# Kernel optimization log

Measured on AMD Instinct MI355X. Metric: run time of the kernel, lower is better.

The kernel has to match this reference:

```python
import jax, jax.numpy as jnp
import numpy as np

B, N, E = 2, 2048, 1024
HQ, HKV = 16, 4           # query heads, kv heads
G = HQ // HKV             # groups (== HKV by construction; required by source einsum)
D = E // HQ               # head_dim = 64
KV_E = D * HKV            # kv projection dim = 256
LN_EPS = 1e-5


def _layernorm(x, g, b):
    mu = jnp.mean(x, axis=-1, keepdims=True)
    var = jnp.mean(jnp.square(x - mu), axis=-1, keepdims=True)
    return (x - mu) * jax.lax.rsqrt(var + LN_EPS) * g + b


def setup_inputs() -> dict:
    key = jax.random.key(0)
    ks = jax.random.split(key, 5)
    s = 0.02
    return {
        "x": jax.random.normal(ks[0], (B, N, E), dtype=jnp.float32),
        "Wq": jax.random.normal(ks[1], (E, E), dtype=jnp.float32) * s,
        "Wk": jax.random.normal(ks[2], (E, KV_E), dtype=jnp.float32) * s,
        "Wv": jax.random.normal(ks[3], (E, KV_E), dtype=jnp.float32) * s,
        "Wout": jax.random.normal(ks[4], (E, E), dtype=jnp.float32) * s,
        "ln_g": jnp.ones((E,), dtype=jnp.float32),
        "ln_b": jnp.zeros((E,), dtype=jnp.float32),
    }


def reference(x, Wq, Wk, Wv, Wout, ln_g, ln_b):
    b, n, _ = x.shape
    # projections
    q = (x @ Wq).reshape(b, n, HQ, D).transpose(0, 2, 1, 3)   # b hq n d
    k = (x @ Wk).reshape(b, n, HKV, D).transpose(0, 2, 1, 3)  # b hkv s d
    v = (x @ Wv).reshape(b, n, HKV, D).transpose(0, 2, 1, 3)  # b hkv s d
    # split query heads: (h g) with h=HKV outer, g=G inner -> b hkv g n d
    q = q.reshape(b, HKV, G, n, D)
    scale = jnp.asarray(np.sqrt(D), dtype=x.dtype)
    scores = jnp.einsum('bhgnd,bhsd->bhgns', q, k) / scale    # b hkv g n s
    causal = jnp.tril(jnp.ones((n, n), dtype=bool))           # n s
    scores = jnp.where(causal[None, None, None, :, :], scores, jnp.asarray(-jnp.inf, x.dtype))
    attn = jax.nn.softmax(scores, axis=-1)                    # b i=hkv j=g n s
    # Faithful to source's mislabeled einsum: value head axis is indexed by the
    # GROUP index j (valid because G == HKV here).
    out = jnp.einsum('bijns,bjsd->bijnd', attn, v)            # b i j n d
    # rearrange 'b g h n d -> b n (h g) d' with g=i, h=j -> merged head order (j, i)
    out = out.transpose(0, 3, 2, 1, 4).reshape(b, n, HQ * D)  # b n E
    out = _layernorm(out, ln_g, ln_b) @ Wout
    # rearrange 'b g h n s -> b n s (h g)' then mean over n
    attn_w = attn.transpose(0, 3, 4, 2, 1).reshape(b, n, n, HQ).mean(axis=1)  # b s HQ
    return (out, attn_w)
```

## Files before the change

### kernel.cpp

```cpp
#include <hip/hip_runtime.h>

#define BB 2
#define NN 2048
#define EE 1024
#define HQH 16
#define DD 64
#define KVE 256
#define QKVW 1536

typedef short bf16x8 __attribute__((ext_vector_type(8)));
typedef short bf16x4 __attribute__((ext_vector_type(4)));
typedef float f32x4 __attribute__((ext_vector_type(4)));
typedef unsigned short u16;
typedef unsigned int u32;

#if __has_builtin(__builtin_amdgcn_exp2f)
#define EXP2(x) __builtin_amdgcn_exp2f(x)
#else
#define EXP2(x) exp2f(x)
#endif

#define QSCALE 0.18033688011112042f

__device__ __forceinline__ u16 f2bf(float f) {
    unsigned u = __float_as_uint(f);
    u += 0x7FFFu + ((u >> 16) & 1u);
    return (u16)(u >> 16);
}
__device__ __forceinline__ float bf2f(u16 h) {
    return __uint_as_float(((unsigned)h) << 16);
}
__device__ __forceinline__ u32 cvtpk(float a, float b) {
    u32 r;
    asm("v_cvt_pk_bf16_f32 %0, %1, %2" : "=v"(r) : "v"(a), "v"(b));
    return r;
}

#define GLOAD_LDS16(gp, lp) __builtin_amdgcn_global_load_lds( \
    (const __attribute__((address_space(1))) unsigned int*)(gp), \
    (__attribute__((address_space(3))) unsigned int*)(lp), 16, 0, 0)

__device__ __forceinline__ bf16x8 xpose8(bf16x8 v, int q) {
    union { bf16x8 v; u32 r[4]; } u_;
    u_.v = v;
    u32 r0 = u_.r[0], r1 = u_.r[1], r2 = u_.r[2], r3 = u_.r[3];
    u32 x, y, t0;
    x = (q & 4) ? r0 : r2;  y = (q & 4) ? r1 : r3;
    x = __shfl_xor(x, 4);   y = __shfl_xor(y, 4);
    if (q & 4) { r0 = x; r1 = y; } else { r2 = x; r3 = y; }
    x = (q & 2) ? r0 : r1;  y = (q & 2) ? r2 : r3;
    x = __shfl_xor(x, 2);   y = __shfl_xor(y, 2);
    if (q & 2) { r0 = x; r2 = y; } else { r1 = x; r3 = y; }
    t0 = __shfl_xor(r0, 1); r0 = (q & 1) ? ((t0 >> 16) | (r0 & 0xFFFF0000u)) : ((r0 & 0xFFFFu) | (t0 << 16));
    t0 = __shfl_xor(r1, 1); r1 = (q & 1) ? ((t0 >> 16) | (r1 & 0xFFFF0000u)) : ((r1 & 0xFFFFu) | (t0 << 16));
    t0 = __shfl_xor(r2, 1); r2 = (q & 1) ? ((t0 >> 16) | (r2 & 0xFFFF0000u)) : ((r2 & 0xFFFFu) | (t0 << 16));
    t0 = __shfl_xor(r3, 1); r3 = (q & 1) ? ((t0 >> 16) | (r3 & 0xFFFF0000u)) : ((r3 & 0xFFFFu) | (t0 << 16));
    u_.r[0] = r0; u_.r[1] = r1; u_.r[2] = r2; u_.r[3] = r3;
    return u_.v;
}

__global__ __launch_bounds__(256)
void conv_bf16(const float* __restrict__ in, u16* __restrict__ out) {
    int i = (blockIdx.x * 256 + threadIdx.x) * 8;
    float4 a = *(const float4*)&in[i];
    float4 b = *(const float4*)&in[i + 4];
    bf16x8 p;
    p[0] = f2bf(a.x); p[1] = f2bf(a.y); p[2] = f2bf(a.z); p[3] = f2bf(a.w);
    p[4] = f2bf(b.x); p[5] = f2bf(b.y); p[6] = f2bf(b.z); p[7] = f2bf(b.w);
    *(bf16x8*)&out[i] = p;
}

__global__ __launch_bounds__(256)
void transp_bf16(const float* __restrict__ W, u16* __restrict__ WT, int Nc) {
    __shared__ float tile[32][33];
    int k0 = blockIdx.x * 32, n0 = blockIdx.y * 32;
    int tx = threadIdx.x & 31, ty = threadIdx.x >> 5;
#pragma unroll
    for (int i = 0; i < 4; ++i)
        tile[ty + i * 8][tx] = W[(size_t)(k0 + ty + i * 8) * Nc + n0 + tx];
    __syncthreads();
#pragma unroll
    for (int i = 0; i < 4; ++i)
        WT[(size_t)(n0 + ty + i * 8) * EE + k0 + tx] = f2bf(tile[tx][ty + i * 8]);
}

__global__ __launch_bounds__(256)
void gemm_mfma(const u16* __restrict__ A, const u16* __restrict__ BT,
               void* __restrict__ C, int K, int ldc, int obf16,
               float qscale, int nq) {
    __shared__ __attribute__((aligned(16))) u16 sA[128 * 64];
    __shared__ __attribute__((aligned(16))) u16 sB[128 * 64];
    int t = threadIdx.x;
    int lane = t & 63, w = t >> 6;
    int wr = w >> 1, wc = w & 1;
    int l15 = lane & 15, lg = lane >> 4;
    int m0 = blockIdx.y * 128, n0 = blockIdx.x * 128;

    f32x4 acc[4][4];
#pragma unroll
    for (int mi = 0; mi < 4; ++mi)
#pragma unroll
        for (int ni = 0; ni < 4; ++ni) acc[mi][ni] = (f32x4){0.f, 0.f, 0.f, 0.f};

    int srow = lane >> 3;
    int schunk = (lane & 7) ^ srow;
    const u16* ga = A + (size_t)(m0 + w * 32 + srow) * K + schunk * 8;
    const u16* gb = BT + (size_t)(n0 + w * 32 + srow) * K + schunk * 8;
    char* lA = (char*)sA + w * 4096;
    char* lB = (char*)sB + w * 4096;

    for (int k0 = 0; k0 < K; k0 += 64) {
#pragma unroll
        for (int i = 0; i < 4; ++i) {
            GLOAD_LDS16(ga + (size_t)i * 8 * K + k0, lA + i * 1024);
            GLOAD_LDS16(gb + (size_t)i * 8 * K + k0, lB + i * 1024);
        }
        __syncthreads();
#pragma unroll
        for (int ks = 0; ks < 2; ++ks) {
            bf16x8 af[4], bfr[4];
#pragma unroll
            for (int mi = 0; mi < 4; ++mi) {
                int row = wr * 64 + mi * 16 + l15;
                af[mi] = *(const bf16x8*)((char*)sA +
                    ((row * 128 + lg * 16 + ks * 64) ^ ((row & 7) << 4)));
            }
#pragma unroll
            for (int ni = 0; ni < 4; ++ni) {
                int row = wc * 64 + ni * 16 + l15;
                bfr[ni] = *(const bf16x8*)((char*)sB +
                    ((row * 128 + lg * 16 + ks * 64) ^ ((row & 7) << 4)));
            }
#pragma unroll
            for (int mi = 0; mi < 4; ++mi)
#pragma unroll
                for (int ni = 0; ni < 4; ++ni)
                    acc[mi][ni] = __builtin_amdgcn_mfma_f32_16x16x32_bf16(
                        af[mi], bfr[ni], acc[mi][ni], 0, 0, 0);
        }
        __syncthreads();
    }

#pragma unroll
    for (int mi = 0; mi < 4; ++mi) {
        int rbase = m0 + wr * 64 + mi * 16 + lg * 4;
#pragma unroll
        for (int ni = 0; ni < 4; ++ni) {
            int col = n0 + wc * 64 + ni * 16 + l15;
            float sc = (col < nq) ? qscale : 1.0f;
            if (obf16) {
                u16* Cb = (u16*)C;
#pragma unroll
                for (int r = 0; r < 4; ++r)
                    Cb[(size_t)(rbase + r) * ldc + col] = f2bf(acc[mi][ni][r] * sc);
            } else {
                float* Cf = (float*)C;
#pragma unroll
                for (int r = 0; r < 4; ++r)
                    Cf[(size_t)(rbase + r) * ldc + col] = acc[mi][ni][r] * sc;
            }
        }
    }
}

__global__ __launch_bounds__(256)
void flash_attn(const u16* __restrict__ QKV, u16* __restrict__ AOb,
                float* __restrict__ mbuf, float* __restrict__ lbuf) {
    __shared__ __attribute__((aligned(16))) u16 sV[2][64 * 64];

    int blk = blockIdx.x;
    int ntile = 15 - (blk & 15);
    int bh = blk >> 4;
    int hq = bh & 15;
    int b = bh >> 4;
    int ih = hq >> 2, jh = hq & 3;
    int hm = jh * 4 + ih;
    int n0 = ntile * 128;
    int t = threadIdx.x;
    int lane = t & 63, w = t >> 6;
    int l15 = lane & 15, lg = lane >> 4;
    int q8 = t & 7;

    const u16* Kg = QKV + (size_t)b * NN * QKVW + EE + ih * DD;
    const u16* Vg = QKV + (size_t)b * NN * QKVW + EE + KVE + jh * DD;

    bf16x8 qf[2][2];
#pragma unroll
    for (int tt = 0; tt < 2; ++tt)
#pragma unroll
        for (int h = 0; h < 2; ++h)
            qf[tt][h] = *(const bf16x8*)(QKV +
                (size_t)(b * NN + n0 + w * 32 + tt * 16 + l15) * QKVW + hq * DD + lg * 8 + h * 32);

    f32x4 o[2][4];
    float mrow[2] = {-1e30f, -1e30f};
    float lrow[2] = {0.f, 0.f};
#pragma unroll
    for (int tt = 0; tt < 2; ++tt)
#pragma unroll
        for (int i = 0; i < 4; ++i) o[tt][i] = (f32x4){0.f, 0.f, 0.f, 0.f};

    int nt = (n0 + 128) >> 6;
    bf16x8 vr[2];
#pragma unroll
    for (int it = 0; it < 2; ++it) {
        int lin = t + it * 256;
        vr[it] = *(const bf16x8*)(Vg + (size_t)((lin >> 6) * 8 + q8) * QKVW + ((lin >> 3) & 7) * 8);
    }
#pragma unroll
    for (int it = 0; it < 2; ++it) {
        int lin = t + it * 256;
        int d = ((lin >> 3) & 7) * 8 + q8;
        int sbase = (lin >> 6) * 8;
        bf16x8 vt = xpose8(vr[it], q8);
        *(bf16x8*)((char*)sV[0] + ((d * 128 + sbase * 2) ^ (q8 << 4))) = vt;
    }

    for (int ti = 0; ti < nt; ++ti) {
        int s0 = ti << 6;
        if (ti + 1 < nt) {
#pragma unroll
            for (int it = 0; it < 2; ++it) {
                int lin = t + it * 256;
                vr[it] = *(const bf16x8*)(Vg +
                    (size_t)(s0 + 64 + (lin >> 6) * 8 + q8) * QKVW + ((lin >> 3) & 7) * 8);
            }
        }
        __syncthreads();
        const char* vb = (const char*)sV[ti & 1];

        f32x4 sf[2][4];
#pragma unroll
        for (int sub = 0; sub < 4; ++sub) {
            const u16* kp = Kg + (size_t)(s0 + sub * 16 + l15) * QKVW + lg * 8;
            bf16x8 k0 = *(const bf16x8*)kp;
            bf16x8 k1 = *(const bf16x8*)(kp + 32);
#pragma unroll
            for (int tt = 0; tt < 2; ++tt) {
                f32x4 z = {0.f, 0.f, 0.f, 0.f};
                z = __builtin_amdgcn_mfma_f32_16x16x32_bf16(k0, qf[tt][0], z, 0, 0, 0);
                sf[tt][sub] = __builtin_amdgcn_mfma_f32_16x16x32_bf16(k1, qf[tt][1], z, 0, 0, 0);
            }
        }

        bf16x8 vf[4][2];
#pragma unroll
        for (int sd = 0; sd < 4; ++sd) {
            int d = sd * 16 + l15;
            int swz = (d & 7) << 4;
#pragma unroll
            for (int f = 0; f < 2; ++f) {
                int aA = (d * 128 + (f * 32 + lg * 4) * 2) ^ swz;
                int aB = (d * 128 + (f * 32 + 16 + lg * 4) * 2) ^ swz;
                bf16x4 lo = *(const bf16x4*)(vb + aA);
                bf16x4 hi = *(const bf16x4*)(vb + aB);
                bf16x8 vv;
                vv[0] = lo[0]; vv[1] = lo[1]; vv[2] = lo[2]; vv[3] = lo[3];
                vv[4] = hi[0]; vv[5] = hi[1]; vv[6] = hi[2]; vv[7] = hi[3];
                vf[sd][f] = vv;
            }
        }

#pragma unroll
        for (int tt = 0; tt < 2; ++tt) {
            int ng_min = n0 + w * 32 + tt * 16;
            int ng = ng_min + l15;
            float mcur = -1e30f;
            if (s0 + 63 > ng_min) {
#pragma unroll
                for (int sub = 0; sub < 4; ++sub)
#pragma unroll
                    for (int r = 0; r < 4; ++r) {
                        int sg = s0 + sub * 16 + lg * 4 + r;
                        float sc = (sg <= ng) ? sf[tt][sub][r] : -1e30f;
                        sf[tt][sub][r] = sc;
                        mcur = fmaxf(mcur, sc);
                    }
            } else {
#pragma unroll
                for (int sub = 0; sub < 4; ++sub)
#pragma unroll
                    for (int r = 0; r < 4; ++r) mcur = fmaxf(mcur, sf[tt][sub][r]);
            }
            mcur = fmaxf(mcur, __shfl_xor(mcur, 16));
            mcur = fmaxf(mcur, __shfl_xor(mcur, 32));

            float mn = mrow[tt];
            if (!__all(mcur <= mn + 8.0f)) {
                mn = fmaxf(mn, mcur);
                float alpha = EXP2(mrow[tt] - mn);
                mrow[tt] = mn;
                lrow[tt] *= alpha;
                float a0 = __shfl(alpha, lg * 4 + 0);
                float a1 = __shfl(alpha, lg * 4 + 1);
                float a2 = __shfl(alpha, lg * 4 + 2);
                float a3 = __shfl(alpha, lg * 4 + 3);
#pragma unroll
                for (int sd = 0; sd < 4; ++sd) {
                    o[tt][sd][0] *= a0; o[tt][sd][1] *= a1;
                    o[tt][sd][2] *= a2; o[tt][sd][3] *= a3;
                }
            }
            float rs = 0.f;
#pragma unroll
            for (int sub = 0; sub < 4; ++sub)
#pragma unroll
                for (int r = 0; r < 4; ++r) {
                    float p = EXP2(sf[tt][sub][r] - mn);
                    sf[tt][sub][r] = p;
                    rs += p;
                }
            rs += __shfl_xor(rs, 16);
            rs += __shfl_xor(rs, 32);
            lrow[tt] += rs;

            union { u32 r[4]; bf16x8 v; } pa0, pa1;
            pa0.r[0] = cvtpk(sf[tt][0][0], sf[tt][0][1]);
            pa0.r[1] = cvtpk(sf[tt][0][2], sf[tt][0][3]);
            pa0.r[2] = cvtpk(sf[tt][1][0], sf[tt][1][1]);
            pa0.r[3] = cvtpk(sf[tt][1][2], sf[tt][1][3]);
            pa1.r[0] = cvtpk(sf[tt][2][0], sf[tt][2][1]);
            pa1.r[1] = cvtpk(sf[tt][2][2], sf[tt][2][3]);
            pa1.r[2] = cvtpk(sf[tt][3][0], sf[tt][3][1]);
            pa1.r[3] = cvtpk(sf[tt][3][2], sf[tt][3][3]);
#pragma unroll
            for (int sd = 0; sd < 4; ++sd) {
                o[tt][sd] = __builtin_amdgcn_mfma_f32_16x16x32_bf16(pa0.v, vf[sd][0], o[tt][sd], 0, 0, 0);
                o[tt][sd] = __builtin_amdgcn_mfma_f32_16x16x32_bf16(pa1.v, vf[sd][1], o[tt][sd], 0, 0, 0);
            }
        }

        if (ti + 1 < nt) {
#pragma unroll
            for (int it = 0; it < 2; ++it) {
                int lin = t + it * 256;
                int d = ((lin >> 3) & 7) * 8 + q8;
                int sbase = (lin >> 6) * 8;
                bf16x8 vt = xpose8(vr[it], q8);
                *(bf16x8*)((char*)sV[(ti + 1) & 1] + ((d * 128 + sbase * 2) ^ (q8 << 4))) = vt;
            }
        }
    }

#pragma unroll
    for (int tt = 0; tt < 2; ++tt) {
        float linv = 1.f / lrow[tt];
        if (lg == 0) {
            int n = n0 + w * 32 + tt * 16 + l15;
            mbuf[(size_t)bh * NN + n] = mrow[tt];
            lbuf[(size_t)bh * NN + n] = linv;
        }
        float i0 = __shfl(linv, lg * 4 + 0);
        float i1 = __shfl(linv, lg * 4 + 1);
        float i2 = __shfl(linv, lg * 4 + 2);
        float i3 = __shfl(linv, lg * 4 + 3);
#pragma unroll
        for (int sd = 0; sd < 4; ++sd) {
            int nb = n0 + w * 32 + tt * 16 + lg * 4;
            size_t base = (size_t)(b * NN + nb) * EE + hm * DD + sd * 16 + l15;
            AOb[base]          = f2bf(o[tt][sd][0] * i0);
            AOb[base + EE]     = f2bf(o[tt][sd][1] * i1);
            AOb[base + 2 * EE] = f2bf(o[tt][sd][2] * i2);
            AOb[base + 3 * EE] = f2bf(o[tt][sd][3] * i3);
        }
    }
}

__global__ __launch_bounds__(256)
void colsum_mfma(const u16* __restrict__ QKV,
                 const float* __restrict__ mbuf, const float* __restrict__ lbuf,
                 float* __restrict__ AW) {
    int blk = blockIdx.x;
    int stile = blk & 15;
    int bh = blk >> 4;
    int hq = bh & 15;
    int b = bh >> 4;
    int ih = hq >> 2, jh = hq & 3;
    int hm = jh * 4 + ih;
    int t = threadIdx.x;
    int lane = t & 63, w = t >> 6;
    int l15 = lane & 15, lg = lane >> 4;
    int sb = stile * 128 + w * 32;

    bf16x8 kf[2][2];
#pragma unroll
    for (int st = 0; st < 2; ++st)
#pragma unroll
        for (int h = 0; h < 2; ++h)
            kf[st][h] = *(const bf16x8*)(QKV +
                (size_t)(b * NN + sb + st * 16 + l15) * QKVW + EE + ih * DD + lg * 8 + h * 32);

    float acc[2][4] = {};
    int nstart = stile * 128;

    const u16* qp0 = QKV + (size_t)(b * NN + nstart + l15) * QKVW + hq * DD + lg * 8;
    bf16x8 q0 = *(const bf16x8*)qp0;
    bf16x8 q1 = *(const bf16x8*)(qp0 + 32);
    float mv = mbuf[(size_t)bh * NN + nstart + l15];
    float li = lbuf[(size_t)bh * NN + nstart + l15];

    for (int nn0 = nstart; nn0 < NN; nn0 += 16) {
        bf16x8 cq0 = q0, cq1 = q1;
        float cmv = mv, cli = li;
        if (nn0 + 16 < NN) {
            const u16* qp = QKV + (size_t)(b * NN + nn0 + 16 + l15) * QKVW + hq * DD + lg * 8;
            q0 = *(const bf16x8*)qp;
            q1 = *(const bf16x8*)(qp + 32);
            mv = mbuf[(size_t)bh * NN + nn0 + 16 + l15];
            li = lbuf[(size_t)bh * NN + nn0 + 16 + l15];
        }
        int n = nn0 + l15;
#pragma unroll
        for (int st = 0; st < 2; ++st) {
            f32x4 z = {0.f, 0.f, 0.f, 0.f};
            z = __builtin_amdgcn_mfma_f32_16x16x32_bf16(kf[st][0], cq0, z, 0, 0, 0);
            z = __builtin_amdgcn_mfma_f32_16x16x32_bf16(kf[st][1], cq1, z, 0, 0, 0);
#pragma unroll
            for (int r = 0; r < 4; ++r) {
                int s = sb + st * 16 + lg * 4 + r;
                float val = EXP2(z[r] - cmv) * cli;
                acc[st][r] += (n >= s) ? val : 0.f;
            }
        }
    }
#pragma unroll
    for (int st = 0; st < 2; ++st)
#pragma unroll
        for (int r = 0; r < 4; ++r) {
            float a = acc[st][r];
            a += __shfl_xor(a, 1);
            a += __shfl_xor(a, 2);
            a += __shfl_xor(a, 4);
            a += __shfl_xor(a, 8);
            if (l15 == 0) {
                int s = sb + st * 16 + lg * 4 + r;
                AW[((size_t)b * NN + s) * HQH + hm] = a * (1.0f / NN);
            }
        }
}

__global__ __launch_bounds__(256)
void layernorm_bf16(u16* __restrict__ X, const float* __restrict__ g,
                    const float* __restrict__ bt) {
    __shared__ float red[256];
    int row = blockIdx.x;
    int t = threadIdx.x;
    u16* xp = X + (size_t)row * EE;
    ushort4 v = *(ushort4*)&xp[t * 4];
    float x0 = bf2f(v.x), x1 = bf2f(v.y), x2 = bf2f(v.z), x3 = bf2f(v.w);
    red[t] = x0 + x1 + x2 + x3;
    __syncthreads();
    for (int off = 128; off > 0; off >>= 1) {
        if (t < off) red[t] += red[t + off];
        __syncthreads();
    }
    float mu = red[0] * (1.f / EE);
    __syncthreads();
    float d0 = x0 - mu, d1 = x1 - mu, d2 = x2 - mu, d3 = x3 - mu;
    red[t] = d0 * d0 + d1 * d1 + d2 * d2 + d3 * d3;
    __syncthreads();
    for (int off = 128; off > 0; off >>= 1) {
        if (t < off) red[t] += red[t + off];
        __syncthreads();
    }
    float rstd = rsqrtf(red[0] * (1.f / EE) + 1e-5f);
    float4 gg = *(const float4*)&g[t * 4];
    float4 bb = *(const float4*)&bt[t * 4];
    ushort4 o;
    o.x = f2bf(d0 * rstd * gg.x + bb.x);
    o.y = f2bf(d1 * rstd * gg.y + bb.y);
    o.z = f2bf(d2 * rstd * gg.z + bb.z);
    o.w = f2bf(d3 * rstd * gg.w + bb.w);
    *(ushort4*)&xp[t * 4] = o;
}

extern "C" void kernel_launch(void* const* d_in, const int* in_sizes, int n_in,
                              void* d_out, int out_size, void* d_ws, size_t ws_size,
                              hipStream_t stream) {
    const float* x    = (const float*)d_in[0];
    const float* Wq   = (const float*)d_in[1];
    const float* Wk   = (const float*)d_in[2];
    const float* Wv   = (const float*)d_in[3];
    const float* Wout = (const float*)d_in[4];
    const float* lng  = (const float*)d_in[5];
    const float* lnb  = (const float*)d_in[6];

    float* out = (float*)d_out;
    float* aw  = out + (size_t)BB * NN * EE;

    u16* Xb    = (u16*)d_ws;
    u16* QKVb  = Xb + (size_t)BB * NN * EE;
    u16* WqkvT = QKVb + (size_t)BB * NN * QKVW;
    u16* WoutT = WqkvT + (size_t)QKVW * EE;
    u16* AOb   = WoutT + (size_t)EE * EE;
    float* mb  = (float*)(AOb + (size_t)BB * NN * EE);
    float* lb  = mb + (size_t)BB * HQH * NN;

    dim3 blk(256);

    conv_bf16<<<BB * NN * EE / 2048, blk, 0, stream>>>(x, Xb);
    transp_bf16<<<dim3(32, 32), blk, 0, stream>>>(Wq, WqkvT, EE);
    transp_bf16<<<dim3(32, 8), blk, 0, stream>>>(Wk, WqkvT + (size_t)EE * EE, KVE);
    transp_bf16<<<dim3(32, 8), blk, 0, stream>>>(Wv, WqkvT + (size_t)(EE + KVE) * EE, KVE);
    transp_bf16<<<dim3(32, 32), blk, 0, stream>>>(Wout, WoutT, EE);

    gemm_mfma<<<dim3(QKVW / 128, BB * NN / 128), blk, 0, stream>>>(
        Xb, WqkvT, QKVb, EE, QKVW, 1, QSCALE, EE);

    int ablocks = BB * HQH * 16;
    flash_attn<<<ablocks, blk, 0, stream>>>(QKVb, AOb, mb, lb);
    colsum_mfma<<<ablocks, blk, 0, stream>>>(QKVb, mb, lb, aw);

    layernorm_bf16<<<BB * NN, blk, 0, stream>>>(AOb, lng, lnb);

    gemm_mfma<<<dim3(EE / 128, BB * NN / 128), blk, 0, stream>>>(
        AOb, WoutT, out, EE, EE, 0, 1.0f, 0);
}
```

Baseline: 298.0 us.

## Use 8 waves per flash-attn block with 16 query rows each, batch colsum loads

The flash attention kernel now launches 512 threads, so each of 8 waves owns 16 query rows instead of 32. This halves per-thread register state and raises wave-level parallelism, and the V tile load is split across more threads. Each wave now loads its own K fragments, so K global traffic per block doubles. MFMA sections are wrapped in s_setprio hints. The colsum kernel now batches four 16-row Q chunks per iteration to increase memory-level parallelism, at the cost of more live registers.

```diff
diff --git a/kernel.cpp b/kernel.cpp
--- a/kernel.cpp
+++ b/kernel.cpp
@@ -163,7 +163,7 @@
     }
 }
 
-__global__ __launch_bounds__(256)
+__global__ __launch_bounds__(512, 4)
 void flash_attn(const u16* __restrict__ QKV, u16* __restrict__ AOb,
                 float* __restrict__ mbuf, float* __restrict__ lbuf) {
     __shared__ __attribute__((aligned(16))) u16 sV[2][64 * 64];
@@ -184,189 +184,160 @@
     const u16* Kg = QKV + (size_t)b * NN * QKVW + EE + ih * DD;
     const u16* Vg = QKV + (size_t)b * NN * QKVW + EE + KVE + jh * DD;
 
-    bf16x8 qf[2][2];
-#pragma unroll
-    for (int tt = 0; tt < 2; ++tt)
-#pragma unroll
-        for (int h = 0; h < 2; ++h)
-            qf[tt][h] = *(const bf16x8*)(QKV +
-                (size_t)(b * NN + n0 + w * 32 + tt * 16 + l15) * QKVW + hq * DD + lg * 8 + h * 32);
-
-    f32x4 o[2][4];
-    float mrow[2] = {-1e30f, -1e30f};
-    float lrow[2] = {0.f, 0.f};
-#pragma unroll
-    for (int tt = 0; tt < 2; ++tt)
-#pragma unroll
-        for (int i = 0; i < 4; ++i) o[tt][i] = (f32x4){0.f, 0.f, 0.f, 0.f};
+    int qrow = n0 + w * 16 + l15;
+    const u16* qp = QKV + (size_t)(b * NN + qrow) * QKVW + hq * DD + lg * 8;
+    bf16x8 qf0 = *(const bf16x8*)qp;
+    bf16x8 qf1 = *(const bf16x8*)(qp + 32);
+
+    f32x4 o[4];
+#pragma unroll
+    for (int i = 0; i < 4; ++i) o[i] = (f32x4){0.f, 0.f, 0.f, 0.f};
+    float mrow = -1e30f, lrow = 0.f;
 
     int nt = (n0 + 128) >> 6;
-    bf16x8 vr[2];
-#pragma unroll
-    for (int it = 0; it < 2; ++it) {
-        int lin = t + it * 256;
-        vr[it] = *(const bf16x8*)(Vg + (size_t)((lin >> 6) * 8 + q8) * QKVW + ((lin >> 3) & 7) * 8);
-    }
-#pragma unroll
-    for (int it = 0; it < 2; ++it) {
-        int lin = t + it * 256;
-        int d = ((lin >> 3) & 7) * 8 + q8;
-        int sbase = (lin >> 6) * 8;
-        bf16x8 vt = xpose8(vr[it], q8);
-        *(bf16x8*)((char*)sV[0] + ((d * 128 + sbase * 2) ^ (q8 << 4))) = vt;
+    int vs = (t >> 6) * 8 + q8;
+    int vd = ((t >> 3) & 7) * 8;
+    int sbase = (t >> 6) * 8;
+    int dres = vd + q8;
+    bf16x8 vr = *(const bf16x8*)(Vg + (size_t)vs * QKVW + vd);
+    {
+        bf16x8 vt = xpose8(vr, q8);
+        *(bf16x8*)((char*)sV[0] + ((dres * 128 + sbase * 2) ^ (q8 << 4))) = vt;
     }
 
     for (int ti = 0; ti < nt; ++ti) {
         int s0 = ti << 6;
-        if (ti + 1 < nt) {
-#pragma unroll
-            for (int it = 0; it < 2; ++it) {
-                int lin = t + it * 256;
-                vr[it] = *(const bf16x8*)(Vg +
-                    (size_t)(s0 + 64 + (lin >> 6) * 8 + q8) * QKVW + ((lin >> 3) & 7) * 8);
-            }
-        }
+        if (ti + 1 < nt)
+            vr = *(const bf16x8*)(Vg + (size_t)(s0 + 64 + vs) * QKVW + vd);
         __syncthreads();
         const char* vb = (const char*)sV[ti & 1];
 
-        f32x4 sf[2][4];
+        bf16x8 k0[4], k1[4];
 #pragma unroll
         for (int sub = 0; sub < 4; ++sub) {
             const u16* kp = Kg + (size_t)(s0 + sub * 16 + l15) * QKVW + lg * 8;
-            bf16x8 k0 = *(const bf16x8*)kp;
-            bf16x8 k1 = *(const bf16x8*)(kp + 32);
-#pragma unroll
-            for (int tt = 0; tt < 2; ++tt) {
-                f32x4 z = {0.f, 0.f, 0.f, 0.f};
-                z = __builtin_amdgcn_mfma_f32_16x16x32_bf16(k0, qf[tt][0], z, 0, 0, 0);
-                sf[tt][sub] = __builtin_amdgcn_mfma_f32_16x16x32_bf16(k1, qf[tt][1], z, 0, 0, 0);
-            }
-        }
-
-        bf16x8 vf[4][2];
+            k0[sub] = *(const bf16x8*)kp;
+            k1[sub] = *(const bf16x8*)(kp + 32);
+        }
+        f32x4 sf[4];
+        __builtin_amdgcn_s_setprio(1);
+#pragma unroll
+        for (int sub = 0; sub < 4; ++sub) {
+            f32x4 z = {0.f, 0.f, 0.f, 0.f};
+            z = __builtin_amdgcn_mfma_f32_16x16x32_bf16(k0[sub], qf0, z, 0, 0, 0);
+            sf[sub] = __builtin_amdgcn_mfma_f32_16x16x32_bf16(k1[sub], qf1, z, 0, 0, 0);
+        }
+        __builtin_amdgcn_s_setprio(0);
+
+        float mcur = -1e30f;
+        if (s0 + 63 > n0 + w * 16) {
+#pragma unroll
+            for (int sub = 0; sub < 4; ++sub)
+#pragma unroll
+                for (int r = 0; r < 4; ++r) {
+                    int sg = s0 + sub * 16 + lg * 4 + r;
+                    float sc = (sg <= qrow) ? sf[sub][r] : -1e30f;
+                    sf[sub][r] = sc;
+                    mcur = fmaxf(mcur, sc);
+                }
+        } else {
+#pragma unroll
+            for (int sub = 0; sub < 4; ++sub)
+#pragma unroll
+                for (int r = 0; r < 4; ++r) mcur = fmaxf(mcur, sf[sub][r]);
+        }
+        mcur = fmaxf(mcur, __shfl_xor(mcur, 16));
+        mcur = fmaxf(mcur, __shfl_xor(mcur, 32));
+
+        float mn = mrow;
+        if (!__all(mcur <= mn + 8.0f)) {
+            mn = fmaxf(mn, mcur);
+            float alpha = EXP2(mrow - mn);
+            mrow = mn;
+            lrow *= alpha;
+            float a0 = __shfl(alpha, lg * 4 + 0);
+            float a1 = __shfl(alpha, lg * 4 + 1);
+            float a2 = __shfl(alpha, lg * 4 + 2);
+            float a3 = __shfl(alpha, lg * 4 + 3);
+#pragma unroll
+            for (int sd = 0; sd < 4; ++sd) {
+                o[sd][0] *= a0; o[sd][1] *= a1;
+                o[sd][2] *= a2; o[sd][3] *= a3;
+            }
+        }
+        float rs = 0.f;
+#pragma unroll
+        for (int sub = 0; sub < 4; ++sub)
+#pragma unroll
+            for (int r = 0; r < 4; ++r) {
+                float p = EXP2(sf[sub][r] - mn);
+                sf[sub][r] = p;
+                rs += p;
+            }
+        rs += __shfl_xor(rs, 16);
+        rs += __shfl_xor(rs, 32);
+        lrow += rs;
+
+        union { u32 r[4]; bf16x8 v; } pa0, pa1;
+        pa0.r[0] = cvtpk(sf[0][0], sf[0][1]);
+        pa0.r[1] = cvtpk(sf[0][2], sf[0][3]);
+        pa0.r[2] = cvtpk(sf[1][0], sf[1][1]);
+        pa0.r[3] = cvtpk(sf[1][2], sf[1][3]);
+        pa1.r[0] = cvtpk(sf[2][0], sf[2][1]);
+        pa1.r[1] = cvtpk(sf[2][2], sf[2][3]);
+        pa1.r[2] = cvtpk(sf[3][0], sf[3][1]);
+        pa1.r[3] = cvtpk(sf[3][2], sf[3][3]);
+
+        __builtin_amdgcn_s_setprio(1);
 #pragma unroll
         for (int sd = 0; sd < 4; ++sd) {
             int d = sd * 16 + l15;
             int swz = (d & 7) << 4;
-#pragma unroll
-            for (int f = 0; f < 2; ++f) {
-                int aA = (d * 128 + (f * 32 + lg * 4) * 2) ^ swz;
-                int aB = (d * 128 + (f * 32 + 16 + lg * 4) * 2) ^ swz;
-                bf16x4 lo = *(const bf16x4*)(vb + aA);
-                bf16x4 hi = *(const bf16x4*)(vb + aB);
-                bf16x8 vv;
-                vv[0] = lo[0]; vv[1] = lo[1]; vv[2] = lo[2]; vv[3] = lo[3];
-                vv[4] = hi[0]; vv[5] = hi[1]; vv[6] = hi[2]; vv[7] = hi[3];
-                vf[sd][f] = vv;
-            }
-        }
-
-#pragma unroll
-        for (int tt = 0; tt < 2; ++tt) {
-            int ng_min = n0 + w * 32 + tt * 16;
-            int ng = ng_min + l15;
-            float mcur = -1e30f;
-            if (s0 + 63 > ng_min) {
-#pragma unroll
-                for (int sub = 0; sub < 4; ++sub)
-#pragma unroll
-                    for (int r = 0; r < 4; ++r) {
-                        int sg = s0 + sub * 16 + lg * 4 + r;
-                        float sc = (sg <= ng) ? sf[tt][sub][r] : -1e30f;
-                        sf[tt][sub][r] = sc;
-                        mcur = fmaxf(mcur, sc);
-                    }
-            } else {
-#pragma unroll
-                for (int sub = 0; sub < 4; ++sub)
-#pragma unroll
-                    for (int r = 0; r < 4; ++r) mcur = fmaxf(mcur, sf[tt][sub][r]);
-            }
-            mcur = fmaxf(mcur, __shfl_xor(mcur, 16));
-            mcur = fmaxf(mcur, __shfl_xor(mcur, 32));
-
-            float mn = mrow[tt];
-            if (!__all(mcur <= mn + 8.0f)) {
-                mn = fmaxf(mn, mcur);
-                float alpha = EXP2(mrow[tt] - mn);
-                mrow[tt] = mn;
-                lrow[tt] *= alpha;
-                float a0 = __shfl(alpha, lg * 4 + 0);
-                float a1 = __shfl(alpha, lg * 4 + 1);
-                float a2 = __shfl(alpha, lg * 4 + 2);
-                float a3 = __shfl(alpha, lg * 4 + 3);
-#pragma unroll
-                for (int sd = 0; sd < 4; ++sd) {
-                    o[tt][sd][0] *= a0; o[tt][sd][1] *= a1;
-                    o[tt][sd][2] *= a2; o[tt][sd][3] *= a3;
-                }
-            }
-            float rs = 0.f;
-#pragma unroll
-            for (int sub = 0; sub < 4; ++sub)
-#pragma unroll
-                for (int r = 0; r < 4; ++r) {
-                    float p = EXP2(sf[tt][sub][r] - mn);
-                    sf[tt][sub][r] = p;
-                    rs += p;
-                }
-            rs += __shfl_xor(rs, 16);
-            rs += __shfl_xor(rs, 32);
-            lrow[tt] += rs;
-
-            union { u32 r[4]; bf16x8 v; } pa0, pa1;
-            pa0.r[0] = cvtpk(sf[tt][0][0], sf[tt][0][1]);
-            pa0.r[1] = cvtpk(sf[tt][0][2], sf[tt][0][3]);
-            pa0.r[2] = cvtpk(sf[tt][1][0], sf[tt][1][1]);
-            pa0.r[3] = cvtpk(sf[tt][1][2], sf[tt][1][3]);
-            pa1.r[0] = cvtpk(sf[tt][2][0], sf[tt][2][1]);
-            pa1.r[1] = cvtpk(sf[tt][2][2], sf[tt][2][3]);
-            pa1.r[2] = cvtpk(sf[tt][3][0], sf[tt][3][1]);
-            pa1.r[3] = cvtpk(sf[tt][3][2], sf[tt][3][3]);
-#pragma unroll
-            for (int sd = 0; sd < 4; ++sd) {
-                o[tt][sd] = __builtin_amdgcn_mfma_f32_16x16x32_bf16(pa0.v, vf[sd][0], o[tt][sd], 0, 0, 0);
-                o[tt][sd] = __builtin_amdgcn_mfma_f32_16x16x32_bf16(pa1.v, vf[sd][1], o[tt][sd], 0, 0, 0);
-            }
-        }
+            int aA = (d * 128 + (lg * 4) * 2) ^ swz;
+            int aB = (d * 128 + (16 + lg * 4) * 2) ^ swz;
+            int aC = (d * 128 + (32 + lg * 4) * 2) ^ swz;
+            int aD = (d * 128 + (48 + lg * 4) * 2) ^ swz;
+            bf16x4 f0lo = *(const bf16x4*)(vb + aA);
+            bf16x4 f0hi = *(const bf16x4*)(vb + aB);
+            bf16x4 f1lo = *(const bf16x4*)(vb + aC);
+            bf16x4 f1hi = *(const bf16x4*)(vb + aD);
+            bf16x8 v0, v1;
+            v0[0] = f0lo[0]; v0[1] = f0lo[1]; v0[2] = f0lo[2]; v0[3] = f0lo[3];
+            v0[4] = f0hi[0]; v0[5] = f0hi[1]; v0[6] = f0hi[2]; v0[7] = f0hi[3];
+            v1[0] = f1lo[0]; v1[1] = f1lo[1]; v1[2] = f1lo[2]; v1[3] = f1lo[3];
+            v1[4] = f1hi[0]; v1[5] = f1hi[1]; v1[6] = f1hi[2]; v1[7] = f1hi[3];
+            o[sd] = __builtin_amdgcn_mfma_f32_16x16x32_bf16(pa0.v, v0, o[sd], 0, 0, 0);
+            o[sd] = __builtin_amdgcn_mfma_f32_16x16x32_bf16(pa1.v, v1, o[sd], 0, 0, 0);
+        }
+        __builtin_amdgcn_s_setprio(0);
 
         if (ti + 1 < nt) {
-#pragma unroll
-            for (int it = 0; it < 2; ++it) {
-                int lin = t + it * 256;
-                int d = ((lin >> 3) & 7) * 8 + q8;
-                int sbase = (lin >> 6) * 8;
-                bf16x8 vt = xpose8(vr[it], q8);
-                *(bf16x8*)((char*)sV[(ti + 1) & 1] + ((d * 128 + sbase * 2) ^ (q8 << 4))) = vt;
-            }
-        }
-    }
-
-#pragma unroll
-    for (int tt = 0; tt < 2; ++tt) {
-        float linv = 1.f / lrow[tt];
-        if (lg == 0) {
-            int n = n0 + w * 32 + tt * 16 + l15;
-            mbuf[(size_t)bh * NN + n] = mrow[tt];
-            lbuf[(size_t)bh * NN + n] = linv;
-        }
-        float i0 = __shfl(linv, lg * 4 + 0);
-        float i1 = __shfl(linv, lg * 4 + 1);
-        float i2 = __shfl(linv, lg * 4 + 2);
-        float i3 = __shfl(linv, lg * 4 + 3);
-#pragma unroll
-        for (int sd = 0; sd < 4; ++sd) {
-            int nb = n0 + w * 32 + tt * 16 + lg * 4;
-            size_t base = (size_t)(b * NN + nb) * EE + hm * DD + sd * 16 + l15;
-            AOb[base]          = f2bf(o[tt][sd][0] * i0);
-            AOb[base + EE]     = f2bf(o[tt][sd][1] * i1);
-            AOb[base + 2 * EE] = f2bf(o[tt][sd][2] * i2);
-            AOb[base + 3 * EE] = f2bf(o[tt][sd][3] * i3);
-        }
-    }
-}
-
-__global__ __launch_bounds__(256)
+            bf16x8 vt = xpose8(vr, q8);
+            *(bf16x8*)((char*)sV[(ti + 1) & 1] + ((dres * 128 + sbase * 2) ^ (q8 << 4))) = vt;
+        }
+    }
+
+    float linv = 1.f / lrow;
+    if (lg == 0) {
+        mbuf[(size_t)bh * NN + qrow] = mrow;
+        lbuf[(size_t)bh * NN + qrow] = linv;
+    }
+    float i0 = __shfl(linv, lg * 4 + 0);
+    float i1 = __shfl(linv, lg * 4 + 1);
+    float i2 = __shfl(linv, lg * 4 + 2);
+    float i3 = __shfl(linv, lg * 4 + 3);
+    int nb = n0 + w * 16 + lg * 4;
+#pragma unroll
+    for (int sd = 0; sd < 4; ++sd) {
+        size_t base = (size_t)(b * NN + nb) * EE + hm * DD + sd * 16 + l15;
+        AOb[base]          = f2bf(o[sd][0] * i0);
+        AOb[base + EE]     = f2bf(o[sd][1] * i1);
+        AOb[base + 2 * EE] = f2bf(o[sd][2] * i2);
+        AOb[base + 3 * EE] = f2bf(o[sd][3] * i3);
+    }
+}
+
+__global__ __launch_bounds__(256, 4)
 void colsum_mfma(const u16* __restrict__ QKV,
                  const float* __restrict__ mbuf, const float* __restrict__ lbuf,
                  float* __restrict__ AW) {
@@ -393,33 +364,33 @@
     float acc[2][4] = {};
     int nstart = stile * 128;
 
-    const u16* qp0 = QKV + (size_t)(b * NN + nstart + l15) * QKVW + hq * DD + lg * 8;
-    bf16x8 q0 = *(const bf16x8*)qp0;
-    bf16x8 q1 = *(const bf16x8*)(qp0 + 32);
-    float mv = mbuf[(size_t)bh * NN + nstart + l15];
-    float li = lbuf[(size_t)bh * NN + nstart + l15];
-
-    for (int nn0 = nstart; nn0 < NN; nn0 += 16) {
-        bf16x8 cq0 = q0, cq1 = q1;
-        float cmv = mv, cli = li;
-        if (nn0 + 16 < NN) {
-            const u16* qp = QKV + (size_t)(b * NN + nn0 + 16 + l15) * QKVW + hq * DD + lg * 8;
-            q0 = *(const bf16x8*)qp;
-            q1 = *(const bf16x8*)(qp + 32);
-            mv = mbuf[(size_t)bh * NN + nn0 + 16 + l15];
-            li = lbuf[(size_t)bh * NN + nn0 + 16 + l15];
-        }
-        int n = nn0 + l15;
-#pragma unroll
-        for (int st = 0; st < 2; ++st) {
-            f32x4 z = {0.f, 0.f, 0.f, 0.f};
-            z = __builtin_amdgcn_mfma_f32_16x16x32_bf16(kf[st][0], cq0, z, 0, 0, 0);
-            z = __builtin_amdgcn_mfma_f32_16x16x32_bf16(kf[st][1], cq1, z, 0, 0, 0);
-#pragma unroll
-            for (int r = 0; r < 4; ++r) {
-                int s = sb + st * 16 + lg * 4 + r;
-                float val = EXP2(z[r] - cmv) * cli;
-                acc[st][r] += (n >= s) ? val : 0.f;
+    for (int nn0 = nstart; nn0 < NN; nn0 += 64) {
+        bf16x8 qc[4][2];
+        float mv[4], lv[4];
+#pragma unroll
+        for (int c = 0; c < 4; ++c) {
+            const u16* qp = QKV + (size_t)(b * NN + nn0 + c * 16 + l15) * QKVW + hq * DD + lg * 8;
+            qc[c][0] = *(const bf16x8*)qp;
+            qc[c][1] = *(const bf16x8*)(qp + 32);
+            mv[c] = mbuf[(size_t)bh * NN + nn0 + c * 16 + l15];
+            lv[c] = lbuf[(size_t)bh * NN + nn0 + c * 16 + l15];
+        }
+#pragma unroll
+        for (int c = 0; c < 4; ++c) {
+            int n = nn0 + c * 16 + l15;
+#pragma unroll
+            for (int st = 0; st < 2; ++st) {
+                f32x4 z = {0.f, 0.f, 0.f, 0.f};
+                __builtin_amdgcn_s_setprio(1);
+                z = __builtin_amdgcn_mfma_f32_16x16x32_bf16(kf[st][0], qc[c][0], z, 0, 0, 0);
+                z = __builtin_amdgcn_mfma_f32_16x16x32_bf16(kf[st][1], qc[c][1], z, 0, 0, 0);
+                __builtin_amdgcn_s_setprio(0);
+#pragma unroll
+                for (int r = 0; r < 4; ++r) {
+                    int s = sb + st * 16 + lg * 4 + r;
+                    float val = EXP2(z[r] - mv[c]) * lv[c];
+                    acc[st][r] += (n >= s) ? val : 0.f;
+                }
             }
         }
     }
@@ -508,7 +479,7 @@
         Xb, WqkvT, QKVb, EE, QKVW, 1, QSCALE, EE);
 
     int ablocks = BB * HQH * 16;
-    flash_attn<<<ablocks, blk, 0, stream>>>(QKVb, AOb, mb, lb);
+    flash_attn<<<ablocks, dim3(512), 0, stream>>>(QKVb, AOb, mb, lb);
     colsum_mfma<<<ablocks, blk, 0, stream>>>(QKVb, mb, lb, aw);
 
     layernorm_bf16<<<BB * NN, blk, 0, stream>>>(AOb, lng, lnb);
```

Measured after the change: 334.3 us. 12.2% more time.
